# Optimization experiments

Hardware: AMD Instinct MI355X
Metric: run time of the kernel (lower is better)

The kernel has to match this reference:

```python
import jax, jax.numpy as jnp
from jax import lax
import numpy as np

T, B, I, H, O = 1000, 256, 128, 512, 32
ALPHA = 20.0 / 100.0  # dt / tau
EXC_RATIO = 0.8
SPARSITY = 0.2


def setup_inputs() -> dict:
    key = jax.random.key(0)
    ks = jax.random.split(key, 8)
    x = jax.random.normal(ks[0], (T, B, I), dtype=jnp.float32)
    w_in = jax.random.normal(ks[1], (H, I), dtype=jnp.float32) * (1.0 / np.sqrt(I))
    b_in = jax.random.uniform(ks[2], (H,), dtype=jnp.float32, minval=-1, maxval=1) / np.sqrt(I)
    w_h = jax.random.normal(ks[3], (H, H), dtype=jnp.float32) * (1.0 / np.sqrt(H))
    b_h = jax.random.uniform(ks[4], (H,), dtype=jnp.float32, minval=-1, maxval=1) / np.sqrt(H)
    n_exc = int(H * EXC_RATIO)
    dale = jnp.where(jnp.arange(H) < n_exc, 1.0, -1.0).astype(jnp.float32)
    # sparse mask: rand < sparsity, diagonal forced True
    sp = (jax.random.uniform(ks[5], (H, H)) < SPARSITY).astype(jnp.float32)
    sparse = jnp.maximum(sp, jnp.eye(H, dtype=jnp.float32))
    fc_w = jax.random.normal(ks[6], (O, H), dtype=jnp.float32) * (1.0 / np.sqrt(H))
    fc_b = jax.random.uniform(ks[7], (O,), dtype=jnp.float32, minval=-1, maxval=1) / np.sqrt(H)
    return {"x": x, "w_in": w_in, "b_in": b_in, "w_h": w_h, "b_h": b_h,
            "dale": dale, "sparse": sparse, "fc_w": fc_w, "fc_b": fc_b}


def reference(x, w_in, b_in, w_h, b_h, dale, sparse, fc_w, fc_b):
    alpha = jnp.float32(ALPHA)
    oma = jnp.float32(1.0 - ALPHA)
    # effective recurrent weight: relu(W) * dale (per presynaptic column) * sparse mask
    w_eff = jax.nn.relu(w_h) * dale[None, :] * sparse  # [H, H]
    # precompute input drive for all timesteps: [T, B, H]
    x_drive = jnp.einsum('tbi,hi->tbh', x, w_in) + b_in

    def step(carry, xd_t):
        state, out = carry
        total = xd_t + out @ w_eff.T + b_h  # [B, H]
        state = state * oma + total * alpha
        out = jax.nn.relu(state)
        return (state, out), out

    init = (jnp.zeros((B, H), x.dtype), jnp.zeros((B, H), x.dtype))
    _, rnn_activity = lax.scan(step, init, x_drive)  # [T, B, H]
    out = jnp.einsum('tbh,oh->tbo', rnn_activity, fc_w) + fc_b  # [T, B, O]
    return out, rnn_activity
```

## Files before the change

kernel.cpp:

```cpp
#include <hip/hip_runtime.h>

#define T_STEPS 1000
#define BATCH   256
#define IN_DIM  128
#define HID     512
#define OUT_DIM 32
#define ALPHA_F 0.2f
#define OMA_F   0.8f
#define MAXNNZ  96
#define BDEPTH  16


__global__ __launch_bounds__(512) void build_rank_kernel(
    const float* __restrict__ w_h, const float* __restrict__ sparse,
    unsigned int* __restrict__ perm, unsigned int* __restrict__ nnzR)
{
    int tid = threadIdx.x;
    __shared__ int cnt_sh[HID];

    const float4* wr4 = (const float4*)(w_h    + tid * HID);
    const float4* sr4 = (const float4*)(sparse + tid * HID);
    int cnt = 0;
    for (int j4 = 0; j4 < HID / 4; j4++) {
        float4 w = wr4[j4];
        float4 s = sr4[j4];
        if (w.x > 0.f && s.x > 0.5f) cnt++;
        if (w.y > 0.f && s.y > 0.5f) cnt++;
        if (w.z > 0.f && s.z > 0.5f) cnt++;
        if (w.w > 0.f && s.w > 0.5f) cnt++;
    }
    int c = min(cnt, MAXNNZ);

    cnt_sh[tid] = c;
    __syncthreads();
    int rank = 0;
    for (int j = 0; j < HID; j++) {
        int cj = cnt_sh[j];
        rank += (cj < c) || (cj == c && j < tid);
    }
    perm[rank] = (unsigned int)tid;
    nnzR[rank] = (unsigned int)c;
}

__global__ __launch_bounds__(64) void fill_kernel(
    const float* __restrict__ w_h, const float* __restrict__ dale,
    const float* __restrict__ sparse,
    const unsigned int* __restrict__ perm, const unsigned int* __restrict__ nnzR,
    float* __restrict__ val_t, unsigned short* __restrict__ idx_t)
{
    int r    = blockIdx.x;
    int lane = threadIdx.x;
    int h = (int)perm[r];
    int c = (int)nnzR[r];

    float*          vout = val_t + r * MAXNNZ;
    unsigned short* iout = idx_t + r * MAXNNZ;

    for (int k = lane; k < MAXNNZ; k += 64)
        if (k >= c) { vout[k] = 0.f; iout[k] = 0; }

    unsigned long long lt = (1ull << lane) - 1ull;
    int pos_base = 0;
#pragma unroll
    for (int ch = 0; ch < 8; ch++) {
        int j = ch * 64 + lane;
        float w = w_h[h * HID + j];
        float s = sparse[h * HID + j];
        bool pred = (w > 0.f) && (s > 0.5f);
        unsigned long long m = __ballot(pred);
        if (pred) {
            int pos = pos_base + (int)__popcll(m & lt);
            if (pos < MAXNNZ) {
                vout[pos] = w * dale[j];
                iout[pos] = (unsigned short)(j * 4);
            }
        }
        pos_base += (int)__popcll(m);
    }
}

__global__ __launch_bounds__(64) void sched_kernel(
    float* __restrict__ val_t, unsigned short* __restrict__ idx_t,
    unsigned int* __restrict__ nnzR)
{
    int w    = blockIdx.x;
    int lane = threadIdx.x;
    int rank = w * 64 + lane;
    int g    = lane >> 5;
    int l32  = lane & 31;

    __shared__ unsigned short entb[64][32][BDEPTH];
    __shared__ unsigned char  cntb[64][32];
    __shared__ unsigned char  outsrc[64][MAXNNZ];
    __shared__ float          vll[64][MAXNNZ];

    int c = (int)nnzR[rank];
    int S = c;
#pragma unroll
    for (int off = 32; off; off >>= 1) S = max(S, __shfl_xor(S, off));

    for (int b = 0; b < 32; b++) cntb[lane][b] = 0;
    for (int e = 0; e < MAXNNZ; e++) {
        vll[lane][e]    = val_t[rank * MAXNNZ + e];
        outsrc[lane][e] = 255;
    }
    unsigned int bm = 0;
    int rem = 0;
    for (int e = 0; e < c; e++) {
        int word = ((int)idx_t[rank * MAXNNZ + e]) >> 2;
        int b = word & 31;
        int k = cntb[lane][b];
        if (k < BDEPTH) {
            entb[lane][b][k] = (unsigned short)((e << 9) | word);
            cntb[lane][b] = (unsigned char)(k + 1);
            bm |= 1u << b;
            rem++;
        }
    }

    for (int s = 0; s < MAXNNZ; s++) {
        int placedWord = -1, placedSrc = -1;
        if (s < S) {
            unsigned int c1 = 0, c2 = 0;
            for (int p = 0; p < 32; p++) {
                int bsel = -1;
                if (l32 == p && rem > 0) {
                    unsigned int a0 = bm & ~c1;
                    unsigned int a1 = bm & c1 & ~c2;
                    bool forced = (rem >= S - s);
                    if (a0)           bsel = __ffs(a0) - 1;
                    else if (a1)      bsel = __ffs(a1) - 1;
                    else if (forced)  bsel = __ffs(bm) - 1;
                }
                int bg = __shfl(bsel, (g << 5) + p);
                if (l32 == p && bsel >= 0) {
                    int k = (int)cntb[lane][bsel] - 1;
                    unsigned short pk = entb[lane][bsel][k];
                    cntb[lane][bsel] = (unsigned char)k;
                    if (k == 0) bm &= ~(1u << bsel);
                    placedWord = pk & 511;
                    placedSrc  = pk >> 9;
                    rem--;
                }
                if (bg >= 0) {
                    if ((c1 >> bg) & 1) c2 |= 1u << bg; else c1 |= 1u << bg;
                }
            }
            unsigned int c1o = (unsigned int)__shfl((int)c1, (g ^ 1) << 5);
            unsigned int freeb = ~(c1 | c1o);
            int pb = freeb ? (__ffs(freeb) - 1) : 0;
            if (placedWord >= 0) {
                idx_t[rank * MAXNNZ + s] = (unsigned short)(placedWord * 4);
                outsrc[lane][s] = (unsigned char)placedSrc;
            } else {
                idx_t[rank * MAXNNZ + s] = (unsigned short)(pb * 4);
            }
        } else {
            idx_t[rank * MAXNNZ + s] = 0;
        }
    }
    nnzR[rank] = (unsigned int)S;

    for (int s = 0; s < MAXNNZ; s++) {
        int src = outsrc[lane][s];
        val_t[rank * MAXNNZ + s] = (src == 255) ? 0.f : vll[lane][src];
    }
}

__global__ __launch_bounds__(256) void trans_kernel(
    const float* __restrict__ w_in, const float* __restrict__ fc_w,
    float* __restrict__ w_inT, float* __restrict__ fcT)
{
    int o = blockIdx.x * 256 + threadIdx.x;
    if (o < IN_DIM * HID) {
        int k = o / HID, n = o % HID;
        w_inT[o] = w_in[n * IN_DIM + k];
    } else {
        int o2 = o - IN_DIM * HID;
        if (o2 < HID * OUT_DIM) {
            int k = o2 / OUT_DIM, oo = o2 % OUT_DIM;
            fcT[o2] = fc_w[oo * HID + k];
        }
    }
}

__global__ __launch_bounds__(256, 4) void ingemm_kernel(
    const float* __restrict__ x, const float* __restrict__ w_inT,
    const float* __restrict__ b_in, const float* __restrict__ b_h,
    float* __restrict__ xd)
{
    __shared__ float xl[256 * 33];
    int tid = threadIdx.x;
    int B  = blockIdx.x;
    int r8 = B & 7;
    int tt = B >> 3;
    int nc = tt & 15;
    int aa = tt >> 4;
    int mb = 8 * aa + r8;
    long m0 = (long)mb * 256;
    int n0 = nc * 32;

    float acc[32];
#pragma unroll
    for (int j = 0; j < 32; j++) acc[j] = b_in[n0 + j] + b_h[n0 + j];

    for (int k0 = 0; k0 < IN_DIM; k0 += 32) {
        __syncthreads();
#pragma unroll
        for (int i = 0; i < 8; i++) {
            int f  = tid + i * 256;
            int rr = f >> 3, cc = f & 7;
            float4 v = *(const float4*)(x + (m0 + rr) * IN_DIM + k0 + cc * 4);
            float* d = &xl[rr * 33 + cc * 4];
            d[0] = v.x; d[1] = v.y; d[2] = v.z; d[3] = v.w;
        }
        __syncthreads();
        const float* xrow = &xl[tid * 33];
#pragma unroll
        for (int kk = 0; kk < 32; kk++) {
            float a = xrow[kk];
            const float* wrow = w_inT + (k0 + kk) * HID + n0;
#pragma unroll
            for (int j = 0; j < 32; j++) acc[j] = fmaf(a, wrow[j], acc[j]);
        }
    }
    float* orow = xd + (m0 + tid) * HID + n0;
#pragma unroll
    for (int j = 0; j < 8; j++)
        *(float4*)(orow + j * 4) =
            make_float4(acc[4*j], acc[4*j+1], acc[4*j+2], acc[4*j+3]);
}


#define PAIR2(base, ii)                                              \
    {                                                                \
        unsigned int pk = idp[ii];                                   \
        float g0 = *(const float*)((base) + (pk & 0xffffu));         \
        float g1 = *(const float*)((base) + (pk >> 16));             \
        a0 = fmaf(val[2*(ii)],     g0, a0);                          \
        a1 = fmaf(val[2*(ii) + 1], g1, a1);                          \
    }

#define CHUNK2(base, c)                                              \
    PAIR2(base, 2*(c)+0) PAIR2(base, 2*(c)+1)

__device__ __forceinline__ float sparse_accum(
    const char* base, const float (&val)[MAXNNZ],
    const unsigned int (&idp)[MAXNNZ / 2], int nch, float a_init)
{
    float a0 = a_init, a1 = 0.f;
    switch (nch) {
        case 24: CHUNK2(base, 23) [[fallthrough]];
        case 23: CHUNK2(base, 22) [[fallthrough]];
        case 22: CHUNK2(base, 21) [[fallthrough]];
        case 21: CHUNK2(base, 20) [[fallthrough]];
        case 20: CHUNK2(base, 19) [[fallthrough]];
        case 19: CHUNK2(base, 18) [[fallthrough]];
        case 18: CHUNK2(base, 17) [[fallthrough]];
        case 17: CHUNK2(base, 16) [[fallthrough]];
        case 16: CHUNK2(base, 15) [[fallthrough]];
        case 15: CHUNK2(base, 14) [[fallthrough]];
        case 14: CHUNK2(base, 13) [[fallthrough]];
        case 13: CHUNK2(base, 12) [[fallthrough]];
        case 12: CHUNK2(base, 11) [[fallthrough]];
        case 11: CHUNK2(base, 10) [[fallthrough]];
        case 10: CHUNK2(base,  9) [[fallthrough]];
        case  9: CHUNK2(base,  8) [[fallthrough]];
        case  8: CHUNK2(base,  7) [[fallthrough]];
        case  7: CHUNK2(base,  6) [[fallthrough]];
        case  6: CHUNK2(base,  5) [[fallthrough]];
        case  5: CHUNK2(base,  4) [[fallthrough]];
        case  4: CHUNK2(base,  3) [[fallthrough]];
        case  3: CHUNK2(base,  2) [[fallthrough]];
        case  2: CHUNK2(base,  1) [[fallthrough]];
        case  1: CHUNK2(base,  0) break;
        default: break;
    }
    return a0 + a1;
}

__global__ __launch_bounds__(512, 2) void scan_kernel(
    float* __restrict__ act_g,
    const float* __restrict__ val_t, const unsigned short* __restrict__ idx_t,
    const unsigned int* __restrict__ perm, const unsigned int* __restrict__ nnzR)
{
    int tid = threadIdx.x;
    int b   = blockIdx.x;
    __shared__ float sbuf[1024];
    sbuf[tid] = 0.f;

    float        val[MAXNNZ];
    unsigned int idp[MAXNNZ / 2];
    {
        const float4* vp = (const float4*)(val_t + tid * MAXNNZ);
#pragma unroll
        for (int i = 0; i < MAXNNZ / 4; i++) {
            float4 v = vp[i];
            val[4*i] = v.x; val[4*i+1] = v.y; val[4*i+2] = v.z; val[4*i+3] = v.w;
        }
        const uint4* ip = (const uint4*)(idx_t + tid * MAXNNZ);
#pragma unroll
        for (int i = 0; i < MAXNNZ / 8; i++) {
            uint4 u = ip[i];
            idp[4*i] = u.x; idp[4*i+1] = u.y; idp[4*i+2] = u.z; idp[4*i+3] = u.w;
        }
    }
    int h = (int)perm[tid];
    int wmax = (int)nnzR[tid | 63];
    wmax = __builtin_amdgcn_readfirstlane(wmax);
    int nch = (wmax + 3) >> 2;

    float state = 0.f;
    int gi = b * HID + h;
    float xdv = act_g[gi];
    const char* sb = (const char*)sbuf;
    __syncthreads();

    for (int t = 0; t < T_STEPS; t += 2) {
        {
            float xn = act_g[gi + BATCH * HID];
            float a = sparse_accum(sb, val, idp, nch, xdv);
            state = state * OMA_F + a * ALPHA_F;
            float act = fmaxf(state, 0.f);
            sbuf[512 + h] = act;
            __syncthreads();
            act_g[gi] = act;
            gi += BATCH * HID;
            xdv = xn;
        }
        {
            int gn = (t < T_STEPS - 2) ? gi + BATCH * HID : gi;
            float xn = act_g[gn];
            float a = sparse_accum(sb + 2048, val, idp, nch, xdv);
            state = state * OMA_F + a * ALPHA_F;
            float act = fmaxf(state, 0.f);
            sbuf[h] = act;
            __syncthreads();
            act_g[gi] = act;
            gi += BATCH * HID;
            xdv = xn;
        }
    }
}

__global__ __launch_bounds__(256, 4) void outgemm_kernel(
    const float* __restrict__ act_g, const float* __restrict__ fcT,
    const float* __restrict__ fc_b, float* __restrict__ out_g)
{
    __shared__ float al[256 * 33];
    int tid = threadIdx.x;
    long m0 = (long)blockIdx.x * 256;

    float acc[32];
#pragma unroll
    for (int o = 0; o < 32; o++) acc[o] = fc_b[o];

    for (int k0 = 0; k0 < HID; k0 += 32) {
        __syncthreads();
#pragma unroll
        for (int i = 0; i < 8; i++) {
            int f  = tid + i * 256;
            int rr = f >> 3, cc = f & 7;
            float4 v = *(const float4*)(act_g + (m0 + rr) * HID + k0 + cc * 4);
            float* d = &al[rr * 33 + cc * 4];
            d[0] = v.x; d[1] = v.y; d[2] = v.z; d[3] = v.w;
        }
        __syncthreads();
        const float* arow = &al[tid * 33];
#pragma unroll
        for (int kk = 0; kk < 32; kk++) {
            float a = arow[kk];
            const float* frow = fcT + (k0 + kk) * OUT_DIM;
#pragma unroll
            for (int o = 0; o < 32; o++) acc[o] = fmaf(a, frow[o], acc[o]);
        }
    }
    float* orow = out_g + (m0 + tid) * OUT_DIM;
#pragma unroll
    for (int j = 0; j < 8; j++)
        *(float4*)(orow + j * 4) =
            make_float4(acc[4*j], acc[4*j+1], acc[4*j+2], acc[4*j+3]);
}

extern "C" void kernel_launch(void* const* d_in, const int* in_sizes, int n_in,
                              void* d_out, int out_size, void* d_ws, size_t ws_size,
                              hipStream_t stream)
{
    const float* x      = (const float*)d_in[0];
    const float* w_in   = (const float*)d_in[1];
    const float* b_in   = (const float*)d_in[2];
    const float* w_h    = (const float*)d_in[3];
    const float* b_h    = (const float*)d_in[4];
    const float* dale   = (const float*)d_in[5];
    const float* sparse = (const float*)d_in[6];
    const float* fc_w   = (const float*)d_in[7];
    const float* fc_b   = (const float*)d_in[8];

    float* out_g = (float*)d_out;
    float* act_g = out_g + (long)T_STEPS * BATCH * OUT_DIM;

    char* ws = (char*)d_ws;
    float*          val_t = (float*)(ws + 0);
    unsigned short* idx_t = (unsigned short*)(ws + 196608);
    unsigned int*   perm  = (unsigned int*)(ws + 294912);
    unsigned int*   nnzR  = (unsigned int*)(ws + 296960);
    float*          w_inT = (float*)(ws + 299008);
    float*          fcT   = (float*)(ws + 561152);

    build_rank_kernel<<<1, 512, 0, stream>>>(w_h, sparse, perm, nnzR);
    fill_kernel<<<HID, 64, 0, stream>>>(w_h, dale, sparse, perm, nnzR, val_t, idx_t);
    sched_kernel<<<8, 64, 0, stream>>>(val_t, idx_t, nnzR);
    trans_kernel<<<320, 256, 0, stream>>>(w_in, fc_w, w_inT, fcT);
    ingemm_kernel<<<16000, 256, 0, stream>>>(x, w_inT, b_in, b_h, act_g);
    scan_kernel<<<256, 512, 0, stream>>>(act_g, val_t, idx_t, perm, nnzR);
    outgemm_kernel<<<1000, 256, 0, stream>>>(act_g, fcT, fc_b, out_g);
}
```

Measured before the change: 2.456 ms.

## Rework sparse-row slot scheduler with ballot-based bank claiming and load-aware schedule length

Replaces the sequential per-lane bank-choice scheduler with a parallel rotated-proposal scheme: each lane proposes a bank, ballots resolve one winner per bank per half-wave, and this repeats for three rounds. The schedule length is now the larger of the maximum row nnz and the maximum per-bank load, and bucket depth rises to 20. The aim is a layout of gathered indices that avoids LDS bank conflicts in the recurrent sparse matvec. The cost is that the schedule may end up longer and the preprocessing logic becomes more complex.

```diff
diff --git a/kernel.cpp b/kernel.cpp
--- a/kernel.cpp
+++ b/kernel.cpp
@@ -8,7 +8,7 @@
 #define ALPHA_F 0.2f
 #define OMA_F   0.8f
 #define MAXNNZ  96
-#define BDEPTH  16
+#define BDEPTH  20
 
 
 __global__ __launch_bounds__(512) void build_rank_kernel(
@@ -88,17 +88,20 @@
     int rank = w * 64 + lane;
     int g    = lane >> 5;
     int l32  = lane & 31;
+    unsigned long long gmask = 0xFFFFFFFFull << (g * 32);
 
     __shared__ unsigned short entb[64][32][BDEPTH];
     __shared__ unsigned char  cntb[64][32];
     __shared__ unsigned char  outsrc[64][MAXNNZ];
     __shared__ float          vll[64][MAXNNZ];
+    __shared__ int            loads[2][32];
 
     int c = (int)nnzR[rank];
-    int S = c;
-#pragma unroll
-    for (int off = 32; off; off >>= 1) S = max(S, __shfl_xor(S, off));
-
+    int cmax = c;
+#pragma unroll
+    for (int off = 32; off; off >>= 1) cmax = max(cmax, __shfl_xor(cmax, off));
+
+    if (lane < 32) { loads[0][lane] = 0; loads[1][lane] = 0; }
     for (int b = 0; b < 32; b++) cntb[lane][b] = 0;
     for (int e = 0; e < MAXNNZ; e++) {
         vll[lane][e]    = val_t[rank * MAXNNZ + e];
@@ -109,7 +112,7 @@
     for (int e = 0; e < c; e++) {
         int word = ((int)idx_t[rank * MAXNNZ + e]) >> 2;
         int b = word & 31;
-        int k = cntb[lane][b];
+        int k = (int)cntb[lane][b];
         if (k < BDEPTH) {
             entb[lane][b][k] = (unsigned short)((e << 9) | word);
             cntb[lane][b] = (unsigned char)(k + 1);
@@ -117,42 +120,57 @@
             rem++;
         }
     }
+    __syncthreads();
+    for (int b = 0; b < 32; b++)
+        if (cntb[lane][b]) atomicAdd(&loads[g][b], (int)cntb[lane][b]);
+    __syncthreads();
+    int ml = 0;
+    if (lane < 32) ml = max(loads[0][lane], loads[1][lane]);
+#pragma unroll
+    for (int off = 32; off; off >>= 1) ml = max(ml, __shfl_xor(ml, off));
+    int S = min(max(cmax, ml), MAXNNZ);
 
     for (int s = 0; s < MAXNNZ; s++) {
-        int placedWord = -1, placedSrc = -1;
         if (s < S) {
-            unsigned int c1 = 0, c2 = 0;
-            for (int p = 0; p < 32; p++) {
-                int bsel = -1;
-                if (l32 == p && rem > 0) {
-                    unsigned int a0 = bm & ~c1;
-                    unsigned int a1 = bm & c1 & ~c2;
-                    bool forced = (rem >= S - s);
-                    if (a0)           bsel = __ffs(a0) - 1;
-                    else if (a1)      bsel = __ffs(a1) - 1;
-                    else if (forced)  bsel = __ffs(bm) - 1;
+            unsigned int claimed = 0;
+            int myb = -1;
+            for (int round = 0; round < 3; round++) {
+                int prop = -1;
+                if (rem > 0 && myb < 0) {
+                    unsigned int avail = bm & ~claimed;
+                    if (avail) {
+                        int rot = (l32 * 5 + s * 3 + round * 11) & 31;
+                        unsigned int av2 = (avail >> rot) | (avail << ((32 - rot) & 31));
+                        int p = __ffs(av2) - 1;
+                        prop = (p + rot) & 31;
+                    }
                 }
-                int bg = __shfl(bsel, (g << 5) + p);
-                if (l32 == p && bsel >= 0) {
-                    int k = (int)cntb[lane][bsel] - 1;
-                    unsigned short pk = entb[lane][bsel][k];
-                    cntb[lane][bsel] = (unsigned char)k;
-                    if (k == 0) bm &= ~(1u << bsel);
-                    placedWord = pk & 511;
-                    placedSrc  = pk >> 9;
-                    rem--;
-                }
-                if (bg >= 0) {
-                    if ((c1 >> bg) & 1) c2 |= 1u << bg; else c1 |= 1u << bg;
+                if (__ballot(prop >= 0) == 0ull) continue;
+                for (int b = 0; b < 32; b++) {
+                    unsigned long long m  = __ballot(prop == b);
+                    unsigned long long mg = m & gmask;
+                    if (mg) {
+                        claimed |= 1u << b;
+                        int winner = 63 - __clzll(mg);
+                        if (lane == winner) myb = b;
+                    }
                 }
             }
-            unsigned int c1o = (unsigned int)__shfl((int)c1, (g ^ 1) << 5);
-            unsigned int freeb = ~(c1 | c1o);
-            int pb = freeb ? (__ffs(freeb) - 1) : 0;
-            if (placedWord >= 0) {
-                idx_t[rank * MAXNNZ + s] = (unsigned short)(placedWord * 4);
-                outsrc[lane][s] = (unsigned char)placedSrc;
+            if (myb < 0 && rem > 0 && rem >= S - s) {
+                unsigned int a = bm & ~claimed;
+                myb = a ? (__ffs(a) - 1) : (__ffs(bm) - 1);
+            }
+            if (myb >= 0) {
+                int k = (int)cntb[lane][myb] - 1;
+                unsigned short pk = entb[lane][myb][k];
+                cntb[lane][myb] = (unsigned char)k;
+                if (k == 0) bm &= ~(1u << myb);
+                outsrc[lane][s] = (unsigned char)(pk >> 9);
+                idx_t[rank * MAXNNZ + s] = (unsigned short)((pk & 511) * 4);
+                rem--;
             } else {
+                unsigned int freeb = ~claimed;
+                int pb = freeb ? (__ffs(freeb) - 1) : 0;
                 idx_t[rank * MAXNNZ + s] = (unsigned short)(pb * 4);
             }
         } else {
```

New measurement: 2.344 ms. 1.05x faster.
